# Optimization experiments

Measured on AMD Instinct MI355X. Metric: run time of the kernel, lower is better.

## Reference

```python
import jax, jax.numpy as jnp
import numpy as np

B, T, D = 8, 2048, 1024
NUM_HEADS = 16
SCALE = 1.0 / np.sqrt(D // NUM_HEADS).astype(np.float32)  # sqrt(d_modal//num_heads), per source


def setup_inputs() -> dict:
    key = jax.random.key(0)
    ks = jax.random.split(key, 7)
    s = 1.0 / np.sqrt(D).astype(np.float32)
    return {
        "x": jax.random.normal(ks[0], (B, T, D), dtype=jnp.float32),
        "Wq_w": jax.random.normal(ks[1], (D, D), dtype=jnp.float32) * s,
        "Wq_b": jax.random.normal(ks[2], (D,), dtype=jnp.float32) * 0.01,
        "Wk_w": jax.random.normal(ks[3], (D, D), dtype=jnp.float32) * s,
        "Wk_b": jax.random.normal(ks[4], (D,), dtype=jnp.float32) * 0.01,
        "Wv_w": jax.random.normal(ks[5], (D, D), dtype=jnp.float32) * s,
        "Wv_b": jax.random.normal(ks[6], (D,), dtype=jnp.float32) * 0.01,
    }


def reference(x, Wq_w, Wq_b, Wk_w, Wk_b, Wv_w, Wv_b):
    # Linear projections (torch nn.Linear: y = x @ W.T + b)
    Q = jnp.einsum('btd,ed->bte', x, Wq_w) + Wq_b
    K = jnp.einsum('btd,ed->bte', x, Wk_w) + Wk_b
    V = jnp.einsum('btd,ed->bte', x, Wv_w) + Wv_b
    # scores [B, T, T], scaled by 1/sqrt(d_modal // num_heads) as in source
    scores = jnp.einsum('bqd,bkd->bqk', Q, K) * SCALE
    causal = jnp.tril(jnp.ones((T, T), dtype=bool))  # tril mask buffer
    scores = jnp.where(causal, scores, -jnp.inf)
    attn = jax.nn.softmax(scores, axis=-1)
    return jnp.einsum('bqk,bkd->bqd', attn, V)
```

## Files before the change

### kernel.cpp

```cpp
#include <hip/hip_runtime.h>


typedef float f32x4 __attribute__((ext_vector_type(4)));
typedef _Float16 half8 __attribute__((ext_vector_type(8)));

#define DEVINL __device__ __forceinline__
static constexpr float ATT_SCALE = 0.125f;

DEVINL void gload_lds16(const _Float16* g, _Float16* l) {
  __builtin_amdgcn_global_load_lds((const __attribute__((address_space(1))) void*)g,
                                   (__attribute__((address_space(3))) void*)l, 16, 0, 0);
}

#define PH_MID() __builtin_amdgcn_s_barrier(); \
    asm volatile("s_waitcnt lgkmcnt(0)" ::: "memory"); \
    __builtin_amdgcn_sched_barrier(0); __builtin_amdgcn_s_setprio(1);
#define PH_END() __builtin_amdgcn_s_setprio(0); __builtin_amdgcn_s_barrier();

template <class GA, class GB>
DEVINL void gemm_core(GA ga, GB gb, int lda, int ldb, int NT,
                      char* ldsb, int tid, f32x4 acc[8][4]) {
  const int l = tid & 63, w = tid >> 6;
  const int wm = w >> 2, wn = w & 3;
  const int lr = l & 15, lk = l >> 4;
  int srow[2], scol[2];
#pragma unroll
  for (int i = 0; i < 2; ++i) {
    const int P = i * 512 + w * 64 + l;
    srow[i] = P >> 3;
    scol[i] = (P & 7) ^ (srow[i] & 7);
  }
  const int ch0 = ((lk ^ (lr & 7)) << 4);
  const int ch1 = (((lk | 4) ^ (lr & 7)) << 4);
  const int abase = lr * 128;
  const int bbase = (wn & 1) * 8192 + lr * 128;

  auto STG = [&](const _Float16* __restrict__ g0, int ld, int bufb, int slot) {
    char* dst = ldsb + bufb * 65536 + slot * 16384;
#pragma unroll
    for (int i = 0; i < 2; ++i)
      gload_lds16(g0 + (size_t)srow[i] * ld + scol[i] * 8,
                  (_Float16*)(dst + i * 8192 + w * 1024));
  };
  auto LDA8 = [&](int bufb, int ih, half8 a[4][2]) {
    const char* sA = ldsb + bufb * 65536 + wm * 16384 + ih * 8192;
#pragma unroll
    for (int i = 0; i < 4; ++i) {
      a[i][0] = *(const half8*)(sA + abase + i * 2048 + ch0);
      a[i][1] = *(const half8*)(sA + abase + i * 2048 + ch1);
    }
  };
  auto LDB4 = [&](int bufb, int jh, half8 bfr[2][2]) {
    const char* sB = ldsb + bufb * 65536 + 32768 + (wn >> 1) * 16384 + jh * 4096;
#pragma unroll
    for (int jj = 0; jj < 2; ++jj) {
      bfr[jj][0] = *(const half8*)(sB + bbase + jj * 2048 + ch0);
      bfr[jj][1] = *(const half8*)(sB + bbase + jj * 2048 + ch1);
    }
  };

  STG(ga(0, 0), lda, 0, 0); STG(ga(0, 1), lda, 0, 1);
  STG(gb(0, 0), ldb, 0, 2); STG(gb(0, 1), ldb, 0, 3);
  STG(gb(1, 0), ldb, 1, 2); STG(gb(1, 1), ldb, 1, 3);
  asm volatile("s_waitcnt vmcnt(4)" ::: "memory");
  __builtin_amdgcn_s_barrier();

  half8 a[4][2], bf0[2][2], bf1[2][2];
  for (int t = 0; t < NT; ++t) {
    const int bufb = t & 1, obuf = bufb ^ 1;
    LDA8(bufb, 0, a);
    LDB4(bufb, 0, bf0);
    if (t + 1 < NT) STG(ga(t + 1, 0), lda, obuf, 0);
    PH_MID();
#pragma unroll
    for (int kk = 0; kk < 2; ++kk)
#pragma unroll
      for (int i = 0; i < 4; ++i)
#pragma unroll
        for (int jj = 0; jj < 2; ++jj)
          acc[i][jj] = __builtin_amdgcn_mfma_f32_16x16x32_f16(a[i][kk], bf0[jj][kk], acc[i][jj], 0, 0, 0);
    PH_END();
    LDB4(bufb, 1, bf1);
    if (t + 1 < NT) STG(ga(t + 1, 1), lda, obuf, 1);
    PH_MID();
#pragma unroll
    for (int kk = 0; kk < 2; ++kk)
#pragma unroll
      for (int i = 0; i < 4; ++i)
#pragma unroll
        for (int jj = 0; jj < 2; ++jj)
          acc[i][2 + jj] = __builtin_amdgcn_mfma_f32_16x16x32_f16(a[i][kk], bf1[jj][kk], acc[i][2 + jj], 0, 0, 0);
    PH_END();
    LDA8(bufb, 1, a);
    if (t + 2 < NT) STG(gb(t + 2, 0), ldb, bufb, 2);
    PH_MID();
#pragma unroll
    for (int kk = 0; kk < 2; ++kk)
#pragma unroll
      for (int i = 0; i < 4; ++i)
#pragma unroll
        for (int jj = 0; jj < 2; ++jj)
          acc[4 + i][jj] = __builtin_amdgcn_mfma_f32_16x16x32_f16(a[i][kk], bf0[jj][kk], acc[4 + i][jj], 0, 0, 0);
    PH_END();
    if (t + 2 < NT) STG(gb(t + 2, 1), ldb, bufb, 3);
    PH_MID();
#pragma unroll
    for (int kk = 0; kk < 2; ++kk)
#pragma unroll
      for (int i = 0; i < 4; ++i)
#pragma unroll
        for (int jj = 0; jj < 2; ++jj)
          acc[4 + i][2 + jj] = __builtin_amdgcn_mfma_f32_16x16x32_f16(a[i][kk], bf1[jj][kk], acc[4 + i][2 + jj], 0, 0, 0);
    __builtin_amdgcn_s_setprio(0);
    if (t + 2 < NT)      { asm volatile("s_waitcnt vmcnt(4)" ::: "memory"); }
    else if (t + 1 < NT) { asm volatile("s_waitcnt vmcnt(0)" ::: "memory"); }
    __builtin_amdgcn_s_barrier();
  }
}

__global__ __launch_bounds__(256) void cvt_f32_f16(const float* __restrict__ in,
                                                   _Float16* __restrict__ out, int n8) {
  int i = blockIdx.x * 256 + threadIdx.x;
  if (i >= n8) return;
  const float4* p = (const float4*)in + (size_t)i * 2;
  float4 v0 = p[0], v1 = p[1];
  half8 h;
  h[0] = (_Float16)v0.x; h[1] = (_Float16)v0.y; h[2] = (_Float16)v0.z; h[3] = (_Float16)v0.w;
  h[4] = (_Float16)v1.x; h[5] = (_Float16)v1.y; h[6] = (_Float16)v1.z; h[7] = (_Float16)v1.w;
  *((half8*)out + i) = h;
}

__global__ __launch_bounds__(512, 2) void gemm_qkv(
    const _Float16* __restrict__ xh, const _Float16* __restrict__ Wqh,
    const _Float16* __restrict__ Wkh, const _Float16* __restrict__ Wvh,
    const float* __restrict__ bq, const float* __restrict__ bk,
    const float* __restrict__ bv, _Float16* __restrict__ Qh,
    _Float16* __restrict__ Kh, _Float16* __restrict__ VT) {
  __shared__ _Float16 lds[65536];
  const int tid = threadIdx.x;
  const int bid = blockIdx.x;
  const int swz = (bid & 7) * 96 + (bid >> 3);
  const int mt = swz / 12, nt = swz % 12;
  const int sel = nt >> 2;
  const _Float16* Wsel = sel == 0 ? Wqh : (sel == 1 ? Wkh : Wvh);
  const float* bsel = sel == 0 ? bq : (sel == 1 ? bk : bv);
  const _Float16* Ab = xh + (size_t)mt * 256 * 1024;
  const _Float16* Bb = Wsel + (size_t)(nt & 3) * 256 * 1024;
  f32x4 acc[8][4] = {};
  auto ga = [&](int t, int h) { return Ab + (size_t)h * 128 * 1024 + t * 64; };
  auto gb = [&](int t, int h) { return Bb + (size_t)h * 128 * 1024 + t * 64; };
  gemm_core(ga, gb, 1024, 1024, 16, (char*)lds, tid, acc);
  const int l = tid & 63, w = tid >> 6;
  const int wm = w >> 2, wn = w & 3;
  const int lr = l & 15, lk = l >> 4;
  const int n0 = (nt & 3) * 256;
  __syncthreads();
#pragma unroll
  for (int ai = 0; ai < 8; ++ai) {
    const int rbase = wm * 128 + (ai >> 2) * 64 + (ai & 3) * 16 + lk * 4;
#pragma unroll
    for (int j = 0; j < 4; ++j) {
      const int col = wn * 64 + j * 16 + lr;
      const float bvv = bsel[n0 + col];
#pragma unroll
      for (int r = 0; r < 4; ++r) {
        const int row = rbase + r;
        const float v = acc[ai][j][r] + bvv;
        if (sel < 2)
          lds[row * 256 + ((col + (row >> 2) * 16) & 255)] = (_Float16)v;
        else
          lds[col * 256 + ((row + (col >> 2) * 16) & 255)] = (_Float16)v;
      }
    }
  }
  __syncthreads();
#pragma unroll
  for (int i = 0; i < 16; ++i) {
    const int c = i * 512 + tid;
    const int row = c >> 5, c8 = c & 31;
    half8 v = *(const half8*)&lds[row * 256 + ((c8 * 8 + (row >> 2) * 16) & 255)];
    if (sel < 2) {
      _Float16* Out = sel == 0 ? Qh : Kh;
      *(half8*)&Out[(size_t)(mt * 256 + row) * 1024 + n0 + c8 * 8] = v;
    } else {
      const int bb = mt >> 3, t0 = (mt & 7) * 256;
      *(half8*)&VT[((size_t)bb * 1024 + n0 + row) * 2048 + t0 + c8 * 8] = v;
    }
  }
}

__global__ __launch_bounds__(512, 2) void gemm_qk(const _Float16* __restrict__ Qh,
                                                  const _Float16* __restrict__ Kh,
                                                  float* __restrict__ Sc) {
  __shared__ _Float16 lds[65536];
  const int tid = threadIdx.x;
  const int idx = blockIdx.x, bb = blockIdx.y;
  int qt = 0;
  while ((qt + 1) * (qt + 2) / 2 <= idx) ++qt;
  const int jt = idx - qt * (qt + 1) / 2;
  const _Float16* Ab = Qh + ((size_t)bb * 2048 + qt * 256) * 1024;
  const _Float16* Bb = Kh + ((size_t)bb * 2048 + jt * 256) * 1024;
  f32x4 acc[8][4] = {};
  auto ga = [&](int t, int h) { return Ab + (size_t)h * 128 * 1024 + t * 64; };
  auto gb = [&](int t, int h) { return Bb + (size_t)h * 128 * 1024 + t * 64; };
  gemm_core(ga, gb, 1024, 1024, 16, (char*)lds, tid, acc);
  const int l = tid & 63, w = tid >> 6;
  const int wm = w >> 2, wn = w & 3;
  const int lr = l & 15, lk = l >> 4;
  float* St = Sc + ((size_t)bb * 36 + idx) * 65536;
  const float NINF = -__builtin_inff();
#pragma unroll
  for (int ai = 0; ai < 8; ++ai) {
    const int rbase = wm * 128 + (ai >> 2) * 64 + (ai & 3) * 16 + lk * 4;
#pragma unroll
    for (int j = 0; j < 4; ++j) {
      const int ck = wn * 64 + j * 16 + lr;
      const int kg = jt * 256 + ck;
#pragma unroll
      for (int r = 0; r < 4; ++r) {
        const int rq = rbase + r;
        const int qg = qt * 256 + rq;
        St[(size_t)rq * 256 + ck] = (kg <= qg) ? acc[ai][j][r] * ATT_SCALE : NINF;
      }
    }
  }
}

__global__ __launch_bounds__(256) void softmax_p(const float* __restrict__ Sc,
                                                 _Float16* __restrict__ Pc) {
  const int l = threadIdx.x & 63;
  const int gid = blockIdx.x * 4 + (threadIdx.x >> 6);
  const int b = gid >> 11, q = gid & 2047;
  const int qt = q >> 8, rq = q & 255;
  const int ntile = qt + 1;
  const size_t base = ((size_t)b * 36 + (size_t)(qt * (qt + 1) / 2)) * 65536 +
                      (size_t)rq * 256 + l * 4;
  float vx[32];
  float m = -__builtin_inff();
#pragma unroll
  for (int c = 0; c < 8; ++c) {
    float4 t = {-__builtin_inff(), -__builtin_inff(), -__builtin_inff(), -__builtin_inff()};
    if (c < ntile) t = *(const float4*)&Sc[base + (size_t)c * 65536];
    vx[4 * c] = t.x; vx[4 * c + 1] = t.y; vx[4 * c + 2] = t.z; vx[4 * c + 3] = t.w;
    m = fmaxf(m, fmaxf(fmaxf(t.x, t.y), fmaxf(t.z, t.w)));
  }
#pragma unroll
  for (int s = 1; s < 64; s <<= 1) m = fmaxf(m, __shfl_xor(m, s, 64));
  float sum = 0.f;
#pragma unroll
  for (int i = 0; i < 32; ++i) { vx[i] = __expf(vx[i] - m); sum += vx[i]; }
#pragma unroll
  for (int s = 1; s < 64; s <<= 1) sum += __shfl_xor(sum, s, 64);
  const float inv = 1.f / sum;
  _Float16* Pb = Pc + base;
#pragma unroll
  for (int c = 0; c < 8; ++c) {
    if (c < ntile) {
      _Float16 tmp[4];
      tmp[0] = (_Float16)(vx[4 * c] * inv);
      tmp[1] = (_Float16)(vx[4 * c + 1] * inv);
      tmp[2] = (_Float16)(vx[4 * c + 2] * inv);
      tmp[3] = (_Float16)(vx[4 * c + 3] * inv);
      *(uint64_t*)&Pb[(size_t)c * 65536] = *(const uint64_t*)tmp;
    }
  }
}

__global__ __launch_bounds__(512, 2) void gemm_pv(const _Float16* __restrict__ Pc,
                                                  const _Float16* __restrict__ VT,
                                                  float* __restrict__ O) {
  __shared__ _Float16 lds[65536];
  const int tid = threadIdx.x;
  const int dt = blockIdx.x, qt = 7 - blockIdx.y, b = blockIdx.z;
  const _Float16* Pb = Pc + ((size_t)b * 36 + (size_t)(qt * (qt + 1) / 2)) * 65536;
  const _Float16* Vb = VT + ((size_t)b * 1024 + dt * 256) * 2048;
  f32x4 acc[8][4] = {};
  auto ga = [&](int t, int h) {
    return Pb + (size_t)(t >> 2) * 65536 + (size_t)h * 128 * 256 + (t & 3) * 64;
  };
  auto gb = [&](int t, int h) { return Vb + (size_t)h * 128 * 2048 + t * 64; };
  gemm_core(ga, gb, 256, 2048, (qt + 1) * 4, (char*)lds, tid, acc);
  const int l = tid & 63, w = tid >> 6;
  const int wm = w >> 2, wn = w & 3;
  const int lr = l & 15, lk = l >> 4;
#pragma unroll
  for (int ai = 0; ai < 8; ++ai) {
    const int rbase = qt * 256 + wm * 128 + (ai >> 2) * 64 + (ai & 3) * 16 + lk * 4;
#pragma unroll
    for (int j = 0; j < 4; ++j) {
      const int cg = dt * 256 + wn * 64 + j * 16 + lr;
#pragma unroll
      for (int r = 0; r < 4; ++r)
        O[((size_t)b * 2048 + rbase + r) * 1024 + cg] = acc[ai][j][r];
    }
  }
}

extern "C" void kernel_launch(void* const* d_in, const int* in_sizes, int n_in,
                              void* d_out, int out_size, void* d_ws, size_t ws_size,
                              hipStream_t stream) {
  const float* x    = (const float*)d_in[0];
  const float* Wq_w = (const float*)d_in[1];
  const float* Wq_b = (const float*)d_in[2];
  const float* Wk_w = (const float*)d_in[3];
  const float* Wk_b = (const float*)d_in[4];
  const float* Wv_w = (const float*)d_in[5];
  const float* Wv_b = (const float*)d_in[6];
  float* out = (float*)d_out;
  char* ws = (char*)d_ws;
  _Float16* xh  = (_Float16*)(ws);
  _Float16* Wqh = (_Float16*)(ws + 33554432);
  _Float16* Wkh = (_Float16*)(ws + 35651584);
  _Float16* Wvh = (_Float16*)(ws + 37748736);
  float*    Sc  = (float*)(ws);
  _Float16* Qh  = (_Float16*)(ws + 75497472);
  _Float16* Kh  = (_Float16*)(ws + 109051904);
  _Float16* Pc  = (_Float16*)(ws + 75497472);
  _Float16* VT  = (_Float16*)(ws + 142606336);

  cvt_f32_f16<<<8192, 256, 0, stream>>>(x, xh, 2097152);
  cvt_f32_f16<<<512, 256, 0, stream>>>(Wq_w, Wqh, 131072);
  cvt_f32_f16<<<512, 256, 0, stream>>>(Wk_w, Wkh, 131072);
  cvt_f32_f16<<<512, 256, 0, stream>>>(Wv_w, Wvh, 131072);
  gemm_qkv<<<768, 512, 0, stream>>>(xh, Wqh, Wkh, Wvh, Wq_b, Wk_b, Wv_b, Qh, Kh, VT);
  gemm_qk<<<dim3(36, 8), 512, 0, stream>>>(Qh, Kh, Sc);
  softmax_p<<<4096, 256, 0, stream>>>(Sc, Pc);
  gemm_pv<<<dim3(4, 8, 8), 512, 0, stream>>>(Pc, VT, out);
}
```

Baseline: 299.3 us.

## Software-pipeline LDS fragment reads across tiles in the shared GEMM core

```diff
diff --git a/kernel.cpp b/kernel.cpp
--- a/kernel.cpp
+++ b/kernel.cpp
@@ -12,14 +12,20 @@
                                    (__attribute__((address_space(3))) void*)l, 16, 0, 0);
 }
 
-#define PH_MID() __builtin_amdgcn_s_barrier(); \
-    asm volatile("s_waitcnt lgkmcnt(0)" ::: "memory"); \
-    __builtin_amdgcn_sched_barrier(0); __builtin_amdgcn_s_setprio(1);
-#define PH_END() __builtin_amdgcn_s_setprio(0); __builtin_amdgcn_s_barrier();
-
-template <class GA, class GB>
-DEVINL void gemm_core(GA ga, GB gb, int lda, int ldb, int NT,
-                      char* ldsb, int tid, f32x4 acc[8][4]) {
+#define SBAR() __builtin_amdgcn_sched_barrier(0)
+#define MM(AOFF, BOFF, ASET, BSET) \
+  _Pragma("unroll") for (int kk_ = 0; kk_ < 2; ++kk_) \
+  _Pragma("unroll") for (int i_ = 0; i_ < 4; ++i_) \
+  _Pragma("unroll") for (int jj_ = 0; jj_ < 2; ++jj_) \
+    acc[(AOFF) + i_][(BOFF) + jj_] = __builtin_amdgcn_mfma_f32_16x16x32_f16( \
+        ASET[i_][kk_], BSET[jj_][kk_], acc[(AOFF) + i_][(BOFF) + jj_], 0, 0, 0);
+#define PHASE_PRE() SBAR(); __builtin_amdgcn_s_barrier(); SBAR(); \
+    __builtin_amdgcn_s_setprio(1)
+#define PHASE_POST() __builtin_amdgcn_s_setprio(0); SBAR(); \
+    __builtin_amdgcn_s_barrier(); SBAR()
+
+template <int LDA, int LDB, class GA, class GB>
+DEVINL void gemm_core(GA ga, GB gb, int NT, char* ldsb, int tid, f32x4 acc[8][4]) {
   const int l = tid & 63, w = tid >> 6;
   const int wm = w >> 2, wn = w & 3;
   const int lr = l & 15, lk = l >> 4;
@@ -31,91 +37,74 @@
     scol[i] = (P & 7) ^ (srow[i] & 7);
   }
   const int ch0 = ((lk ^ (lr & 7)) << 4);
-  const int ch1 = (((lk | 4) ^ (lr & 7)) << 4);
+  const int ch1 = (((lk + 4) ^ (lr & 7)) << 4);
   const int abase = lr * 128;
   const int bbase = (wn & 1) * 8192 + lr * 128;
 
-  auto STG = [&](const _Float16* __restrict__ g0, int ld, int bufb, int slot) {
-    char* dst = ldsb + bufb * 65536 + slot * 16384;
+  half8 aA[4][2], aB[4][2], bA[2][2], bB[2][2];
+
+  auto STGA = [&](int t, int h, int bufb) {
+    const _Float16* g0 = ga(t, h);
+    char* dst = ldsb + bufb * 65536 + h * 16384;
 #pragma unroll
     for (int i = 0; i < 2; ++i)
-      gload_lds16(g0 + (size_t)srow[i] * ld + scol[i] * 8,
+      gload_lds16(g0 + (size_t)srow[i] * LDA + scol[i] * 8,
                   (_Float16*)(dst + i * 8192 + w * 1024));
   };
-  auto LDA8 = [&](int bufb, int ih, half8 a[4][2]) {
+  auto STGB = [&](int t, int h, int bufb) {
+    const _Float16* g0 = gb(t, h);
+    char* dst = ldsb + bufb * 65536 + 32768 + h * 16384;
+#pragma unroll
+    for (int i = 0; i < 2; ++i)
+      gload_lds16(g0 + (size_t)srow[i] * LDB + scol[i] * 8,
+                  (_Float16*)(dst + i * 8192 + w * 1024));
+  };
+  auto RDA = [&](int bufb, int ih, half8 d[4][2]) {
     const char* sA = ldsb + bufb * 65536 + wm * 16384 + ih * 8192;
 #pragma unroll
     for (int i = 0; i < 4; ++i) {
-      a[i][0] = *(const half8*)(sA + abase + i * 2048 + ch0);
-      a[i][1] = *(const half8*)(sA + abase + i * 2048 + ch1);
-    }
-  };
-  auto LDB4 = [&](int bufb, int jh, half8 bfr[2][2]) {
+      d[i][0] = *(const half8*)(sA + abase + i * 2048 + ch0);
+      d[i][1] = *(const half8*)(sA + abase + i * 2048 + ch1);
+    }
+  };
+  auto RDB = [&](int bufb, int jh, half8 d[2][2]) {
     const char* sB = ldsb + bufb * 65536 + 32768 + (wn >> 1) * 16384 + jh * 4096;
 #pragma unroll
     for (int jj = 0; jj < 2; ++jj) {
-      bfr[jj][0] = *(const half8*)(sB + bbase + jj * 2048 + ch0);
-      bfr[jj][1] = *(const half8*)(sB + bbase + jj * 2048 + ch1);
-    }
-  };
-
-  STG(ga(0, 0), lda, 0, 0); STG(ga(0, 1), lda, 0, 1);
-  STG(gb(0, 0), ldb, 0, 2); STG(gb(0, 1), ldb, 0, 3);
-  STG(gb(1, 0), ldb, 1, 2); STG(gb(1, 1), ldb, 1, 3);
+      d[jj][0] = *(const half8*)(sB + bbase + jj * 2048 + ch0);
+      d[jj][1] = *(const half8*)(sB + bbase + jj * 2048 + ch1);
+    }
+  };
+
+  auto tile = [&](int t, bool stA, bool stB) {
+    const int bufb = t & 1, obuf = bufb ^ 1;
+    RDB(bufb, 1, bB);
+    if (stA) STGA(t + 1, 0, obuf);
+    PHASE_PRE(); MM(0, 0, aA, bA); PHASE_POST();
+    RDA(bufb, 1, aB);
+    if (stA) STGA(t + 1, 1, obuf);
+    PHASE_PRE(); MM(0, 2, aA, bB); PHASE_POST();
+    if (stB) STGB(t + 2, 0, bufb);
+    SBAR(); __builtin_amdgcn_s_barrier(); SBAR();
+    __builtin_amdgcn_s_setprio(1);
+    MM(4, 0, aB, bA);
+    __builtin_amdgcn_s_setprio(0); SBAR();
+    if (stB) { asm volatile("s_waitcnt vmcnt(2)" ::: "memory"); }
+    else     { asm volatile("s_waitcnt vmcnt(0)" ::: "memory"); }
+    __builtin_amdgcn_s_barrier(); SBAR();
+    if (stA) { RDA(obuf, 0, aA); RDB(obuf, 0, bA); }
+    if (stB) STGB(t + 2, 1, bufb);
+    PHASE_PRE(); MM(4, 2, aB, bB); PHASE_POST();
+  };
+
+  STGA(0, 0, 0); STGA(0, 1, 0); STGB(0, 0, 0); STGB(0, 1, 0);
+  STGB(1, 0, 1); STGB(1, 1, 1);
   asm volatile("s_waitcnt vmcnt(4)" ::: "memory");
-  __builtin_amdgcn_s_barrier();
-
-  half8 a[4][2], bf0[2][2], bf1[2][2];
-  for (int t = 0; t < NT; ++t) {
-    const int bufb = t & 1, obuf = bufb ^ 1;
-    LDA8(bufb, 0, a);
-    LDB4(bufb, 0, bf0);
-    if (t + 1 < NT) STG(ga(t + 1, 0), lda, obuf, 0);
-    PH_MID();
-#pragma unroll
-    for (int kk = 0; kk < 2; ++kk)
-#pragma unroll
-      for (int i = 0; i < 4; ++i)
-#pragma unroll
-        for (int jj = 0; jj < 2; ++jj)
-          acc[i][jj] = __builtin_amdgcn_mfma_f32_16x16x32_f16(a[i][kk], bf0[jj][kk], acc[i][jj], 0, 0, 0);
-    PH_END();
-    LDB4(bufb, 1, bf1);
-    if (t + 1 < NT) STG(ga(t + 1, 1), lda, obuf, 1);
-    PH_MID();
-#pragma unroll
-    for (int kk = 0; kk < 2; ++kk)
-#pragma unroll
-      for (int i = 0; i < 4; ++i)
-#pragma unroll
-        for (int jj = 0; jj < 2; ++jj)
-          acc[i][2 + jj] = __builtin_amdgcn_mfma_f32_16x16x32_f16(a[i][kk], bf1[jj][kk], acc[i][2 + jj], 0, 0, 0);
-    PH_END();
-    LDA8(bufb, 1, a);
-    if (t + 2 < NT) STG(gb(t + 2, 0), ldb, bufb, 2);
-    PH_MID();
-#pragma unroll
-    for (int kk = 0; kk < 2; ++kk)
-#pragma unroll
-      for (int i = 0; i < 4; ++i)
-#pragma unroll
-        for (int jj = 0; jj < 2; ++jj)
-          acc[4 + i][jj] = __builtin_amdgcn_mfma_f32_16x16x32_f16(a[i][kk], bf0[jj][kk], acc[4 + i][jj], 0, 0, 0);
-    PH_END();
-    if (t + 2 < NT) STG(gb(t + 2, 1), ldb, bufb, 3);
-    PH_MID();
-#pragma unroll
-    for (int kk = 0; kk < 2; ++kk)
-#pragma unroll
-      for (int i = 0; i < 4; ++i)
-#pragma unroll
-        for (int jj = 0; jj < 2; ++jj)
-          acc[4 + i][2 + jj] = __builtin_amdgcn_mfma_f32_16x16x32_f16(a[i][kk], bf1[jj][kk], acc[4 + i][2 + jj], 0, 0, 0);
-    __builtin_amdgcn_s_setprio(0);
-    if (t + 2 < NT)      { asm volatile("s_waitcnt vmcnt(4)" ::: "memory"); }
-    else if (t + 1 < NT) { asm volatile("s_waitcnt vmcnt(0)" ::: "memory"); }
-    __builtin_amdgcn_s_barrier();
-  }
+  __builtin_amdgcn_s_barrier(); SBAR();
+  RDA(0, 0, aA); RDB(0, 0, bA);
+  for (int t = 0; t < NT - 2; ++t) tile(t, true, true);
+  tile(NT - 2, true, false);
+  tile(NT - 1, false, false);
 }
 
 __global__ __launch_bounds__(256) void cvt_f32_f16(const float* __restrict__ in,
@@ -149,7 +138,7 @@
   f32x4 acc[8][4] = {};
   auto ga = [&](int t, int h) { return Ab + (size_t)h * 128 * 1024 + t * 64; };
   auto gb = [&](int t, int h) { return Bb + (size_t)h * 128 * 1024 + t * 64; };
-  gemm_core(ga, gb, 1024, 1024, 16, (char*)lds, tid, acc);
+  gemm_core<1024, 1024>(ga, gb, 16, (char*)lds, tid, acc);
   const int l = tid & 63, w = tid >> 6;
   const int wm = w >> 2, wn = w & 3;
   const int lr = l & 15, lk = l >> 4;
@@ -203,7 +192,7 @@
   f32x4 acc[8][4] = {};
   auto ga = [&](int t, int h) { return Ab + (size_t)h * 128 * 1024 + t * 64; };
   auto gb = [&](int t, int h) { return Bb + (size_t)h * 128 * 1024 + t * 64; };
-  gemm_core(ga, gb, 1024, 1024, 16, (char*)lds, tid, acc);
+  gemm_core<1024, 1024>(ga, gb, 16, (char*)lds, tid, acc);
   const int l = tid & 63, w = tid >> 6;
   const int wm = w >> 2, wn = w & 3;
   const int lr = l & 15, lk = l >> 4;
@@ -279,7 +268,7 @@
     return Pb + (size_t)(t >> 2) * 65536 + (size_t)h * 128 * 256 + (t & 3) * 64;
   };
   auto gb = [&](int t, int h) { return Vb + (size_t)h * 128 * 2048 + t * 64; };
-  gemm_core(ga, gb, 256, 2048, (qt + 1) * 4, (char*)lds, tid, acc);
+  gemm_core<256, 2048>(ga, gb, (qt + 1) * 4, (char*)lds, tid, acc);
   const int l = tid & 63, w = tid >> 6;
   const int wm = w >> 2, wn = w & 3;
   const int lr = l & 15, lk = l >> 4;
```

New measurement: 294.7 us. About the same (-1.5%).
